# Optimization experiments

Hardware: AMD Instinct MI355X
Metric: run time of the kernel (lower is better)

The kernel has to match this reference:

```python
import jax, jax.numpy as jnp
import numpy as np

N_NODES = 100000
N_EDGES = 3200000
N_FEAT = 500
HIDDEN = 128
N_CLASSES = 64
K_LAYERS = 10
ALPHA = 0.1


def setup_inputs() -> dict:
    key = jax.random.key(0)
    k_x, k_e, k_w1, k_b1, k_w2, k_b2 = jax.random.split(key, 6)
    x = jax.random.normal(k_x, (N_NODES, N_FEAT), dtype=jnp.float32)
    edge_index = jax.random.randint(k_e, (2, N_EDGES), 0, N_NODES, dtype=jnp.int64)
    # Linear layers (torch nn.Linear default init ~ U(-1/sqrt(fan_in), 1/sqrt(fan_in)))
    s1 = 1.0 / np.sqrt(N_FEAT)
    s2 = 1.0 / np.sqrt(HIDDEN)
    W1 = jax.random.uniform(k_w1, (N_FEAT, HIDDEN), jnp.float32, -s1, s1)
    b1 = jax.random.uniform(k_b1, (HIDDEN,), jnp.float32, -s1, s1)
    W2 = jax.random.uniform(k_w2, (HIDDEN, N_CLASSES), jnp.float32, -s2, s2)
    b2 = jax.random.uniform(k_b2, (N_CLASSES,), jnp.float32, -s2, s2)
    return {"x": x, "edge_index": edge_index, "W1": W1, "b1": b1, "W2": W2, "b2": b2}


def reference(x, edge_index, W1, b1, W2, b2):
    n = x.shape[0]
    # MLP: Linear -> ReLU -> Linear
    h = jnp.maximum(x @ W1 + b1, 0.0) @ W2 + b2  # [N, C]

    # GCN symmetric normalization with self-loops (PyG APPNP / gcn_norm)
    loops = jnp.arange(n, dtype=edge_index.dtype)
    src = jnp.concatenate([edge_index[0], loops])
    dst = jnp.concatenate([edge_index[1], loops])
    deg = jax.ops.segment_sum(jnp.ones_like(dst, dtype=h.dtype), dst, num_segments=n)
    dinv = jnp.where(deg > 0, jax.lax.rsqrt(deg), 0.0)
    norm = dinv[src] * dinv[dst]  # [E+N]

    h0 = h

    def step(z, _):
        msgs = z[src] * norm[:, None]                       # gather over edges
        agg = jax.ops.segment_sum(msgs, dst, num_segments=n)  # scatter-add
        z_new = (1.0 - ALPHA) * agg + ALPHA * h0
        return z_new, None

    z, _ = jax.lax.scan(step, h0, None, length=K_LAYERS)
    return jax.nn.softmax(z, axis=1)
```

## Files before the change

### kernel.cpp

```cpp
#include <hip/hip_runtime.h>
#include <hip/hip_bf16.h>
#include <hip/hip_fp16.h>

#define N_NODES   100000
#define N_EDGES   3200000
#define N_FEAT    500
#define HIDDEN    128
#define N_CLASSES 64
#define K_LAYERS  10
#define NBUCK     98

typedef __attribute__((ext_vector_type(4))) float f32x4;
typedef __attribute__((ext_vector_type(8))) _Float16 f16x8;

__device__ inline float2 h2f2(unsigned u) {
  __half2 h = *(__half2*)&u;
  return make_float2(__low2float(h), __high2float(h));
}
__device__ inline unsigned f2h2(float a, float b) {
  __half2 h = __floats2half2_rn(a, b);
  return *(unsigned*)&h;
}


__global__ __launch_bounds__(256) void bucket_count_k(const int* __restrict__ dst,
                                                      int* __restrict__ bucket_cnt) {
  __shared__ int h[128];
  int t = threadIdx.x;
  if (t < 128) h[t] = 0;
  __syncthreads();
  for (int e = blockIdx.x * 256 + t; e < N_EDGES; e += gridDim.x * 256)
    atomicAdd(&h[dst[e] >> 10], 1);
  __syncthreads();
  if (t < 128 && h[t]) atomicAdd(&bucket_cnt[t], h[t]);
}

__global__ __launch_bounds__(128) void bucket_scan_k(const int* __restrict__ bucket_cnt,
                                                     int* __restrict__ bucket_base,
                                                     int* __restrict__ bcur,
                                                     int* __restrict__ offs) {
  __shared__ int sm[128];
  int t = threadIdx.x;
  int c = bucket_cnt[t];
  sm[t] = c;
  __syncthreads();
  for (int d = 1; d < 128; d <<= 1) {
    int v = (t >= d) ? sm[t - d] : 0;
    __syncthreads();
    sm[t] += v;
    __syncthreads();
  }
  int ex = sm[t] - c;
  bucket_base[t] = ex;
  bcur[t] = ex;
  if (t == 127) bucket_base[128] = ex + c;
  if (t == 0) offs[N_NODES] = N_EDGES;
}

#define BIN_CHUNK 12800
__global__ __launch_bounds__(256) void bin_scatter_k(const int* __restrict__ src,
                                                     const int* __restrict__ dst,
                                                     int* __restrict__ bcur,
                                                     int* __restrict__ binned) {
  __shared__ int h[128];
  __shared__ int hbase[128];
  int t = threadIdx.x;
  int e0 = blockIdx.x * BIN_CHUNK;
  int e1 = min(e0 + BIN_CHUNK, N_EDGES);
  if (t < 128) h[t] = 0;
  __syncthreads();
  for (int e = e0 + t; e < e1; e += 256) atomicAdd(&h[dst[e] >> 10], 1);
  __syncthreads();
  if (t < 128) {
    int c = h[t];
    hbase[t] = c ? atomicAdd(&bcur[t], c) : 0;
  }
  __syncthreads();
  if (t < 128) h[t] = 0;
  __syncthreads();
  for (int e = e0 + t; e < e1; e += 256) {
    int d = dst[e];
    int b = d >> 10;
    int pos = hbase[b] + atomicAdd(&h[b], 1);
    binned[pos] = (src[e] & 0x1FFFF) | ((d & 1023) << 17);
  }
}

__global__ __launch_bounds__(256) void bucket_fill_k(const int* __restrict__ binned,
                                                     const int* __restrict__ bucket_base,
                                                     int* __restrict__ offs,
                                                     float* __restrict__ dinv,
                                                     int* __restrict__ csr4) {
  __shared__ int cnt[1024];
  __shared__ int tsum[256];
  int b = blockIdx.x;
  int base = bucket_base[b];
  int nE = bucket_base[b + 1] - base;
  int node0 = b << 10;
  int nN = min(1024, N_NODES - node0);
  int t = threadIdx.x;
  #pragma unroll
  for (int i = 0; i < 4; ++i) cnt[t + i * 256] = 0;
  __syncthreads();
  for (int i = t; i < nE; i += 256) atomicAdd(&cnt[binned[base + i] >> 17], 1);
  __syncthreads();
  int c0 = cnt[4 * t], c1 = cnt[4 * t + 1], c2 = cnt[4 * t + 2], c3 = cnt[4 * t + 3];
  int s = c0 + c1 + c2 + c3;
  tsum[t] = s;
  __syncthreads();
  for (int d = 1; d < 256; d <<= 1) {
    int v = (t >= d) ? tsum[t - d] : 0;
    __syncthreads();
    tsum[t] += v;
    __syncthreads();
  }
  int run = tsum[t] - s;
  int p0 = run, p1 = run + c0, p2 = p1 + c1, p3 = p2 + c2;
  if (4 * t + 0 < nN) { offs[node0 + 4 * t + 0] = base + p0; dinv[node0 + 4 * t + 0] = rsqrtf(c0 + 1.f); }
  if (4 * t + 1 < nN) { offs[node0 + 4 * t + 1] = base + p1; dinv[node0 + 4 * t + 1] = rsqrtf(c1 + 1.f); }
  if (4 * t + 2 < nN) { offs[node0 + 4 * t + 2] = base + p2; dinv[node0 + 4 * t + 2] = rsqrtf(c2 + 1.f); }
  if (4 * t + 3 < nN) { offs[node0 + 4 * t + 3] = base + p3; dinv[node0 + 4 * t + 3] = rsqrtf(c3 + 1.f); }
  __syncthreads();
  cnt[4 * t] = p0; cnt[4 * t + 1] = p1; cnt[4 * t + 2] = p2; cnt[4 * t + 3] = p3;
  __syncthreads();
  for (int i = t; i < nE; i += 256) {
    int rec = binned[base + i];
    int p = base + atomicAdd(&cnt[rec >> 17], 1);
    csr4[p] = rec & 0x1FFFF;
  }
}

__global__ void prep_wsw_k(const float* __restrict__ W, ushort* __restrict__ Bsw,
                           int KTOT, int BN, int KPAD) {
  int g = blockIdx.x * 256 + threadIdx.x;
  if (g >= BN * KPAD) return;
  int chunk = BN * 64;
  int s = g / chunk;
  int r = g - s * chunk;
  int c = r >> 6;
  int q = r & 63;
  int X = (q >> 3) ^ (c & 7);
  int e = q & 7;
  int k = s * 64 + X * 8 + e;
  float v = (k < KTOT) ? W[(size_t)k * BN + c] : 0.f;
  _Float16 hv = (_Float16)v;
  Bsw[g] = *(ushort*)&hv;
}

template<int BN, int KTOT, int KPAD, bool RELU, bool A16, bool C16>
__device__ __forceinline__ void gemm_core(const void* Ain, const ushort* Bsw,
                                          const float* bias, void* Cout, int M) {
  constexpr int BK = 64;
  constexpr int NS = KPAD / BK;
  constexpr int NF = BN / 16;
  constexpr int CHUNK = BN * BK;
  constexpr int NL = CHUNK * 2 / (16 * 256);
  __shared__ __align__(16) ushort Bl[2][CHUNK];

  int tid = threadIdx.x;
  int lane = tid & 63, w = tid >> 6;
  int lrow = lane & 15, lg = lane >> 4;
  int row0 = blockIdx.x * 128 + w * 32;

  const float* A32 = (const float*)Ain;
  const ushort* Ah = (const ushort*)Ain;

  f32x4 acc[2][NF];
  #pragma unroll
  for (int m = 0; m < 2; ++m)
    #pragma unroll
    for (int n = 0; n < NF; ++n) acc[m][n] = (f32x4){0.f, 0.f, 0.f, 0.f};

  #define STAGE(s, buf)                                                   \
    {                                                                     \
      const ushort* gp = Bsw + (size_t)(s) * CHUNK;                       \
      _Pragma("unroll")                                                   \
      for (int i = 0; i < NL; ++i) {                                      \
        int o = (tid + i * 256) * 8;                                      \
        __builtin_amdgcn_global_load_lds(gp + o, &Bl[buf][o], 16, 0, 0);  \
      }                                                                   \
    }

  STAGE(0, 0);
  asm volatile("s_waitcnt vmcnt(0)" ::: "memory");
  __syncthreads();

  #pragma unroll 1
  for (int s = 0; s < NS; ++s) {
    int cur = s & 1;
    if (s + 1 < NS) STAGE(s + 1, cur ^ 1);
    int kc = s * BK;
    #pragma unroll
    for (int ks = 0; ks < 2; ++ks) {
      f16x8 af[2];
      #pragma unroll
      for (int m = 0; m < 2; ++m) {
        int r = row0 + m * 16 + lrow;
        int rc = r < M ? r : M - 1;
        int k0 = kc + ks * 32 + lg * 8;
        if (A16) {
          af[m] = *(const f16x8*)(Ah + (size_t)rc * KPAD + k0);
        } else {
          const float* ap = A32 + (size_t)rc * KTOT + k0;
          f16x8 h;
          if (k0 + 7 < KTOT) {
            float4 f0 = *(const float4*)ap;
            float4 f1 = *(const float4*)(ap + 4);
            h[0] = (_Float16)f0.x; h[1] = (_Float16)f0.y;
            h[2] = (_Float16)f0.z; h[3] = (_Float16)f0.w;
            h[4] = (_Float16)f1.x; h[5] = (_Float16)f1.y;
            h[6] = (_Float16)f1.z; h[7] = (_Float16)f1.w;
          } else {
            #pragma unroll
            for (int e = 0; e < 8; ++e)
              h[e] = (_Float16)((k0 + e < KTOT) ? ap[e] : 0.f);
          }
          af[m] = h;
        }
      }
      #pragma unroll
      for (int n = 0; n < NF; ++n) {
        int c = n * 16 + lrow;
        int ad = c * 64 + ((((ks << 2) + lg) ^ (c & 7)) << 3);
        f16x8 bf = *(const f16x8*)(&Bl[cur][ad]);
        #pragma unroll
        for (int m = 0; m < 2; ++m)
          acc[m][n] = __builtin_amdgcn_mfma_f32_16x16x32_f16(af[m], bf, acc[m][n], 0, 0, 0);
      }
    }
    asm volatile("s_waitcnt vmcnt(0)" ::: "memory");
    __syncthreads();
  }
  #undef STAGE

  #pragma unroll
  for (int m = 0; m < 2; ++m)
    #pragma unroll
    for (int n = 0; n < NF; ++n) {
      int c = n * 16 + lrow;
      float bb = bias[c];
      #pragma unroll
      for (int r4 = 0; r4 < 4; ++r4) {
        int grow = row0 + m * 16 + lg * 4 + r4;
        if (grow < M) {
          float v = acc[m][n][r4] + bb;
          if (RELU) v = fmaxf(v, 0.f);
          if (C16) {
            _Float16 hv = (_Float16)v;
            ((ushort*)Cout)[(size_t)grow * BN + c] = *(ushort*)&hv;
          } else {
            ((float*)Cout)[(size_t)grow * BN + c] = v;
          }
        }
      }
    }
}

__global__ __launch_bounds__(256, 2) void gemm1_k(const float* __restrict__ A,
                                                  const ushort* __restrict__ Bsw,
                                                  const float* __restrict__ bias,
                                                  ushort* __restrict__ C, int M) {
  gemm_core<128, 500, 512, true, false, true>(A, Bsw, bias, C, M);
}
__global__ __launch_bounds__(256, 2) void gemm2_k(const ushort* __restrict__ A,
                                                  const ushort* __restrict__ Bsw,
                                                  const float* __restrict__ bias,
                                                  float* __restrict__ C, int M) {
  gemm_core<64, 128, 128, false, true, false>(A, Bsw, bias, C, M);
}

__global__ __launch_bounds__(256) void conv_y0_k(const float* __restrict__ h0,
                                                 const float* __restrict__ dinv,
                                                 uint4* __restrict__ y16,
                                                 uint4* __restrict__ h16) {
  int j = blockIdx.x * 256 + threadIdx.x;
  if (j >= N_NODES * 8) return;
  int node = j >> 3;
  float dv = dinv[node];
  const float4* hp = (const float4*)(h0 + (size_t)j * 8);
  float4 a = hp[0], b = hp[1];
  y16[j] = make_uint4(f2h2(dv * a.x, dv * a.y), f2h2(dv * a.z, dv * a.w),
                      f2h2(dv * b.x, dv * b.y), f2h2(dv * b.z, dv * b.w));
  h16[j] = make_uint4(f2h2(a.x, a.y), f2h2(a.z, a.w),
                      f2h2(b.x, b.y), f2h2(b.z, b.w));
}

template<bool OUT32>
__global__ __launch_bounds__(256) void prop_k(const uint4* __restrict__ yin,
                                              void* __restrict__ out,
                                              const uint4* __restrict__ h016,
                                              const float* __restrict__ h0f,
                                              const float* __restrict__ dinv,
                                              const int* __restrict__ offs,
                                              const int* __restrict__ csr4) {
  int lane = threadIdx.x & 63;
  int wid = threadIdx.x >> 6;
  int node = (blockIdx.x << 2) + wid;
  if (node >= N_NODES) return;
  int grp = lane >> 3;
  int lc = lane & 7;

  float acc[8];
  #pragma unroll
  for (int i = 0; i < 8; ++i) acc[i] = 0.f;

  int beg = offs[node], end = offs[node + 1];
  for (int e = beg; e < end; e += 64) {
    int s = (e + lane < end) ? csr4[e + lane] : N_NODES;
    int cnt = min(64, end - e);
    for (int j = 0; j < cnt; j += 32) {
      int sr[4];
      uint4 g[4];
      #pragma unroll
      for (int q = 0; q < 4; ++q) sr[q] = __shfl(s, j + 8 * q + grp);
      #pragma unroll
      for (int q = 0; q < 4; ++q) g[q] = yin[(size_t)sr[q] * 8 + lc];
      #pragma unroll
      for (int q = 0; q < 4; ++q) {
        float2 p0 = h2f2(g[q].x), p1 = h2f2(g[q].y);
        float2 p2 = h2f2(g[q].z), p3 = h2f2(g[q].w);
        acc[0] += p0.x; acc[1] += p0.y; acc[2] += p1.x; acc[3] += p1.y;
        acc[4] += p2.x; acc[5] += p2.y; acc[6] += p3.x; acc[7] += p3.y;
      }
    }
  }
  #pragma unroll
  for (int off = 8; off <= 32; off <<= 1)
    #pragma unroll
    for (int i = 0; i < 8; ++i) acc[i] += __shfl_xor(acc[i], off);

  if (grp == 0) {
    uint4 gs = yin[(size_t)node * 8 + lc];
    {
      float2 p0 = h2f2(gs.x), p1 = h2f2(gs.y), p2 = h2f2(gs.z), p3 = h2f2(gs.w);
      acc[0] += p0.x; acc[1] += p0.y; acc[2] += p1.x; acc[3] += p1.y;
      acc[4] += p2.x; acc[5] += p2.y; acc[6] += p3.x; acc[7] += p3.y;
    }
    float dv = dinv[node];
    float z[8];
    if (OUT32) {
      const float4* hp = (const float4*)(h0f + (size_t)node * 64 + lc * 8);
      float4 hA = hp[0], hB = hp[1];
      z[0] = 0.9f * dv * acc[0] + 0.1f * hA.x;
      z[1] = 0.9f * dv * acc[1] + 0.1f * hA.y;
      z[2] = 0.9f * dv * acc[2] + 0.1f * hA.z;
      z[3] = 0.9f * dv * acc[3] + 0.1f * hA.w;
      z[4] = 0.9f * dv * acc[4] + 0.1f * hB.x;
      z[5] = 0.9f * dv * acc[5] + 0.1f * hB.y;
      z[6] = 0.9f * dv * acc[6] + 0.1f * hB.z;
      z[7] = 0.9f * dv * acc[7] + 0.1f * hB.w;
      float4* zp = (float4*)out + (size_t)node * 16 + lc * 2;
      zp[0] = make_float4(z[0], z[1], z[2], z[3]);
      zp[1] = make_float4(z[4], z[5], z[6], z[7]);
    } else {
      uint4 hh = h016[(size_t)node * 8 + lc];
      float2 h0p = h2f2(hh.x), h1p = h2f2(hh.y), h2p = h2f2(hh.z), h3p = h2f2(hh.w);
      z[0] = 0.9f * dv * acc[0] + 0.1f * h0p.x;
      z[1] = 0.9f * dv * acc[1] + 0.1f * h0p.y;
      z[2] = 0.9f * dv * acc[2] + 0.1f * h1p.x;
      z[3] = 0.9f * dv * acc[3] + 0.1f * h1p.y;
      z[4] = 0.9f * dv * acc[4] + 0.1f * h2p.x;
      z[5] = 0.9f * dv * acc[5] + 0.1f * h2p.y;
      z[6] = 0.9f * dv * acc[6] + 0.1f * h3p.x;
      z[7] = 0.9f * dv * acc[7] + 0.1f * h3p.y;
      ((uint4*)out)[(size_t)node * 8 + lc] =
          make_uint4(f2h2(dv * z[0], dv * z[1]), f2h2(dv * z[2], dv * z[3]),
                     f2h2(dv * z[4], dv * z[5]), f2h2(dv * z[6], dv * z[7]));
    }
  }
}

__global__ __launch_bounds__(256) void softmax_k(const float* __restrict__ z,
                                                 float* __restrict__ out) {
  int lane = threadIdx.x & 63;
  int row = (blockIdx.x * 256 + threadIdx.x) >> 6;
  if (row >= N_NODES) return;
  float v = z[(size_t)row * 64 + lane];
  float m = v;
  #pragma unroll
  for (int o = 32; o > 0; o >>= 1) m = fmaxf(m, __shfl_xor(m, o));
  float ev = __expf(v - m);
  float s = ev;
  #pragma unroll
  for (int o = 32; o > 0; o >>= 1) s += __shfl_xor(s, o);
  out[(size_t)row * 64 + lane] = ev / s;
}

extern "C" void kernel_launch(void* const* d_in, const int* in_sizes, int n_in,
                              void* d_out, int out_size, void* d_ws, size_t ws_size,
                              hipStream_t stream) {
  const float* x  = (const float*)d_in[0];
  const int*   ei = (const int*)d_in[1];
  const float* W1 = (const float*)d_in[2];
  const float* b1 = (const float*)d_in[3];
  const float* W2 = (const float*)d_in[4];
  const float* b2 = (const float*)d_in[5];
  const int* src = ei;
  const int* dst = ei + N_EDGES;

  char* w = (char*)d_ws;
  int*    csr4  = (int*)w;
  ushort* H     = (ushort*)(w + 12800000);
  uint4*  yA    = (uint4*)(w + 12800000);
  uint4*  yB    = (uint4*)(w + 25700000);
  float*  zF32  = (float*)(w + 38600000);
  int*    binned = (int*)(w + 38600000);
  float*  dinv  = (float*)(w + 64500000);
  int*    offs  = (int*)(w + 65000000);
  int*    bucket_cnt  = (int*)(w + 66000000);
  int*    bucket_base = (int*)(w + 66002048);
  int*    bcur        = (int*)(w + 66004096);
  ushort* w1sw  = (ushort*)(w + 66500000);
  ushort* w2sw  = (ushort*)(w + 66700000);
  uint4*  h016  = (uint4*)(w + 70000000);
  float* h0 = (float*)d_out;

  hipMemsetAsync(bucket_cnt, 0, 128 * 4, stream);

  bucket_count_k<<<512, 256, 0, stream>>>(dst, bucket_cnt);
  bucket_scan_k<<<1, 128, 0, stream>>>(bucket_cnt, bucket_base, bcur, offs);
  bin_scatter_k<<<N_EDGES / BIN_CHUNK, 256, 0, stream>>>(src, dst, bcur, binned);
  bucket_fill_k<<<NBUCK, 256, 0, stream>>>(binned, bucket_base, offs, dinv, csr4);

  prep_wsw_k<<<(128 * 512 + 255) / 256, 256, 0, stream>>>(W1, w1sw, 500, 128, 512);
  prep_wsw_k<<<(64 * 128 + 255) / 256, 256, 0, stream>>>(W2, w2sw, 128, 64, 128);
  gemm1_k<<<(N_NODES + 127) / 128, 256, 0, stream>>>(x, w1sw, b1, H, N_NODES);
  gemm2_k<<<(N_NODES + 127) / 128, 256, 0, stream>>>(H, w2sw, b2, h0, N_NODES);

  hipMemsetAsync((char*)yA + (size_t)N_NODES * 128, 0, 128, stream);
  hipMemsetAsync((char*)yB + (size_t)N_NODES * 128, 0, 128, stream);

  conv_y0_k<<<(N_NODES * 8 + 255) / 256, 256, 0, stream>>>(h0, dinv, yA, h016);

  const uint4* zi = yA;
  uint4* zo = yB;
  for (int it = 0; it < K_LAYERS - 1; ++it) {
    prop_k<false><<<(N_NODES + 3) / 4, 256, 0, stream>>>(
        zi, (void*)zo, h016, h0, dinv, offs, csr4);
    zi = zo;
    zo = (zo == yA) ? yB : yA;
  }
  prop_k<true><<<(N_NODES + 3) / 4, 256, 0, stream>>>(
      zi, (void*)zF32, h016, h0, dinv, offs, csr4);

  softmax_k<<<(N_NODES * 64) / 256, 256, 0, stream>>>(zF32, (float*)d_out);
}
```

Before: 975.6 us.

## Fuse fp16 conversion into GEMM2 epilogue and softmax into final propagation

The GEMM2 epilogue now writes the fp32 h0 plus the fp16 dinv-scaled and unscaled copies directly, and zeroes the pad rows itself. This removes the conv_y0 kernel and two memsets. The last propagation step computes the row softmax in registers across 8 lanes and writes straight to the output, which drops the fp32 z buffer and the separate softmax kernel. In exchange the GEMM epilogue issues more scattered 2-byte stores, and the final step reads h0 from d_out while overwriting it, which is safe only because each node's slice is read before it is written by the same lanes.

Result: no change. 958.9 us (-1.7%).

```diff
diff --git a/kernel.cpp b/kernel.cpp
--- a/kernel.cpp
+++ b/kernel.cpp
@@ -147,9 +147,11 @@
   Bsw[g] = *(ushort*)&hv;
 }
 
-template<int BN, int KTOT, int KPAD, bool RELU, bool A16, bool C16>
+template<int BN, int KTOT, int KPAD, bool RELU, bool A16, int CMODE>
 __device__ __forceinline__ void gemm_core(const void* Ain, const ushort* Bsw,
-                                          const float* bias, void* Cout, int M) {
+                                          const float* bias, void* Cout, int M,
+                                          const float* dinv, ushort* Yp,
+                                          ushort* Hp) {
   constexpr int BK = 64;
   constexpr int NS = KPAD / BK;
   constexpr int NF = BN / 16;
@@ -245,11 +247,16 @@
         if (grow < M) {
           float v = acc[m][n][r4] + bb;
           if (RELU) v = fmaxf(v, 0.f);
-          if (C16) {
+          if (CMODE == 1) {
             _Float16 hv = (_Float16)v;
             ((ushort*)Cout)[(size_t)grow * BN + c] = *(ushort*)&hv;
           } else {
+            float dv = dinv[grow];
             ((float*)Cout)[(size_t)grow * BN + c] = v;
+            _Float16 hy = (_Float16)(dv * v);
+            _Float16 hh = (_Float16)v;
+            Yp[(size_t)grow * BN + c] = *(ushort*)&hy;
+            Hp[(size_t)grow * BN + c] = *(ushort*)&hh;
           }
         }
       }
@@ -260,32 +267,26 @@
                                                   const ushort* __restrict__ Bsw,
                                                   const float* __restrict__ bias,
                                                   ushort* __restrict__ C, int M) {
-  gemm_core<128, 500, 512, true, false, true>(A, Bsw, bias, C, M);
+  gemm_core<128, 500, 512, true, false, 1>(A, Bsw, bias, C, M, nullptr, nullptr, nullptr);
 }
 __global__ __launch_bounds__(256, 2) void gemm2_k(const ushort* __restrict__ A,
                                                   const ushort* __restrict__ Bsw,
                                                   const float* __restrict__ bias,
-                                                  float* __restrict__ C, int M) {
-  gemm_core<64, 128, 128, false, true, false>(A, Bsw, bias, C, M);
-}
-
-__global__ __launch_bounds__(256) void conv_y0_k(const float* __restrict__ h0,
-                                                 const float* __restrict__ dinv,
-                                                 uint4* __restrict__ y16,
-                                                 uint4* __restrict__ h16) {
-  int j = blockIdx.x * 256 + threadIdx.x;
-  if (j >= N_NODES * 8) return;
-  int node = j >> 3;
-  float dv = dinv[node];
-  const float4* hp = (const float4*)(h0 + (size_t)j * 8);
-  float4 a = hp[0], b = hp[1];
-  y16[j] = make_uint4(f2h2(dv * a.x, dv * a.y), f2h2(dv * a.z, dv * a.w),
-                      f2h2(dv * b.x, dv * b.y), f2h2(dv * b.z, dv * b.w));
-  h16[j] = make_uint4(f2h2(a.x, a.y), f2h2(a.z, a.w),
-                      f2h2(b.x, b.y), f2h2(b.z, b.w));
-}
-
-template<bool OUT32>
+                                                  float* __restrict__ C, int M,
+                                                  const float* __restrict__ dinv,
+                                                  ushort* __restrict__ Yp,
+                                                  ushort* __restrict__ Hp,
+                                                  uint4* __restrict__ padA,
+                                                  uint4* __restrict__ padB) {
+  if (blockIdx.x == 0 && threadIdx.x < 16) {
+    uint4 z = make_uint4(0, 0, 0, 0);
+    if (threadIdx.x < 8) padA[threadIdx.x] = z;
+    else padB[threadIdx.x - 8] = z;
+  }
+  gemm_core<64, 128, 128, false, true, 2>(A, Bsw, bias, C, M, dinv, Yp, Hp);
+}
+
+template<bool SMAX>
 __global__ __launch_bounds__(256) void prop_k(const uint4* __restrict__ yin,
                                               void* __restrict__ out,
                                               const uint4* __restrict__ h016,
@@ -338,7 +339,7 @@
     }
     float dv = dinv[node];
     float z[8];
-    if (OUT32) {
+    if (SMAX) {
       const float4* hp = (const float4*)(h0f + (size_t)node * 64 + lc * 8);
       float4 hA = hp[0], hB = hp[1];
       z[0] = 0.9f * dv * acc[0] + 0.1f * hA.x;
@@ -349,9 +350,20 @@
       z[5] = 0.9f * dv * acc[5] + 0.1f * hB.y;
       z[6] = 0.9f * dv * acc[6] + 0.1f * hB.z;
       z[7] = 0.9f * dv * acc[7] + 0.1f * hB.w;
+      float m = z[0];
+      #pragma unroll
+      for (int i = 1; i < 8; ++i) m = fmaxf(m, z[i]);
+      #pragma unroll
+      for (int o = 1; o <= 4; o <<= 1) m = fmaxf(m, __shfl_xor(m, o));
+      float ev[8], ssum = 0.f;
+      #pragma unroll
+      for (int i = 0; i < 8; ++i) { ev[i] = __expf(z[i] - m); ssum += ev[i]; }
+      #pragma unroll
+      for (int o = 1; o <= 4; o <<= 1) ssum += __shfl_xor(ssum, o);
+      float inv = 1.f / ssum;
       float4* zp = (float4*)out + (size_t)node * 16 + lc * 2;
-      zp[0] = make_float4(z[0], z[1], z[2], z[3]);
-      zp[1] = make_float4(z[4], z[5], z[6], z[7]);
+      zp[0] = make_float4(ev[0] * inv, ev[1] * inv, ev[2] * inv, ev[3] * inv);
+      zp[1] = make_float4(ev[4] * inv, ev[5] * inv, ev[6] * inv, ev[7] * inv);
     } else {
       uint4 hh = h016[(size_t)node * 8 + lc];
       float2 h0p = h2f2(hh.x), h1p = h2f2(hh.y), h2p = h2f2(hh.z), h3p = h2f2(hh.w);
@@ -370,22 +382,6 @@
   }
 }
 
-__global__ __launch_bounds__(256) void softmax_k(const float* __restrict__ z,
-                                                 float* __restrict__ out) {
-  int lane = threadIdx.x & 63;
-  int row = (blockIdx.x * 256 + threadIdx.x) >> 6;
-  if (row >= N_NODES) return;
-  float v = z[(size_t)row * 64 + lane];
-  float m = v;
-  #pragma unroll
-  for (int o = 32; o > 0; o >>= 1) m = fmaxf(m, __shfl_xor(m, o));
-  float ev = __expf(v - m);
-  float s = ev;
-  #pragma unroll
-  for (int o = 32; o > 0; o >>= 1) s += __shfl_xor(s, o);
-  out[(size_t)row * 64 + lane] = ev / s;
-}
-
 extern "C" void kernel_launch(void* const* d_in, const int* in_sizes, int n_in,
                               void* d_out, int out_size, void* d_ws, size_t ws_size,
                               hipStream_t stream) {
@@ -401,9 +397,6 @@
   char* w = (char*)d_ws;
   int*    csr4  = (int*)w;
   ushort* H     = (ushort*)(w + 12800000);
-  uint4*  yA    = (uint4*)(w + 12800000);
-  uint4*  yB    = (uint4*)(w + 25700000);
-  float*  zF32  = (float*)(w + 38600000);
   int*    binned = (int*)(w + 38600000);
   float*  dinv  = (float*)(w + 64500000);
   int*    offs  = (int*)(w + 65000000);
@@ -413,6 +406,8 @@
   ushort* w1sw  = (ushort*)(w + 66500000);
   ushort* w2sw  = (ushort*)(w + 66700000);
   uint4*  h016  = (uint4*)(w + 70000000);
+  uint4*  yA    = (uint4*)(w + 83000000);
+  uint4*  yB    = (uint4*)(w + 96000000);
   float* h0 = (float*)d_out;
 
   hipMemsetAsync(bucket_cnt, 0, 128 * 4, stream);
@@ -425,23 +420,18 @@
   prep_wsw_k<<<(128 * 512 + 255) / 256, 256, 0, stream>>>(W1, w1sw, 500, 128, 512);
   prep_wsw_k<<<(64 * 128 + 255) / 256, 256, 0, stream>>>(W2, w2sw, 128, 64, 128);
   gemm1_k<<<(N_NODES + 127) / 128, 256, 0, stream>>>(x, w1sw, b1, H, N_NODES);
-  gemm2_k<<<(N_NODES + 127) / 128, 256, 0, stream>>>(H, w2sw, b2, h0, N_NODES);
-
-  hipMemsetAsync((char*)yA + (size_t)N_NODES * 128, 0, 128, stream);
-  hipMemsetAsync((char*)yB + (size_t)N_NODES * 128, 0, 128, stream);
-
-  conv_y0_k<<<(N_NODES * 8 + 255) / 256, 256, 0, stream>>>(h0, dinv, yA, h016);
+  gemm2_k<<<(N_NODES + 127) / 128, 256, 0, stream>>>(
+      H, w2sw, b2, h0, N_NODES, dinv, (ushort*)yA, (ushort*)h016,
+      yA + (size_t)N_NODES * 8, yB + (size_t)N_NODES * 8);
 
   const uint4* zi = yA;
   uint4* zo = yB;
   for (int it = 0; it < K_LAYERS - 1; ++it) {
     prop_k<false><<<(N_NODES + 3) / 4, 256, 0, stream>>>(
-        zi, (void*)zo, h016, h0, dinv, offs, csr4);
+        zi, (void*)zo, h016, nullptr, dinv, offs, csr4);
     zi = zo;
     zo = (zo == yA) ? yB : yA;
   }
   prop_k<true><<<(N_NODES + 3) / 4, 256, 0, stream>>>(
-      zi, (void*)zF32, h016, h0, dinv, offs, csr4);
-
-  softmax_k<<<(N_NODES * 64) / 256, 256, 0, stream>>>(zF32, (float*)d_out);
-}
+      zi, d_out, h016, (const float*)d_out, dinv, offs, csr4);
+}
```
